# Kernel optimization log

Measured on AMD Instinct MI355X. Metric: run time of the kernel, lower is better.

Reference implementation:

```python
import jax, jax.numpy as jnp
import numpy as np

N_NODES = 100000

def sage_conv(x, edge_index, Wl, bl, Wr):
    # PyG SAGEConv, aggr='add', normalize=False:
    #   out = lin_l(sum_{j in N(i)} x_j) + lin_r(x_i)
    src, dst = edge_index[0], edge_index[1]
    agg = jax.ops.segment_sum(x[src], dst, num_segments=N_NODES)  # [N, F]
    return agg @ Wl.T + bl + x @ Wr.T


def setup_inputs() -> dict:
    key = jax.random.key(0)
    ks = jax.random.split(key, 7)
    F_IN, HID, C, E = 128, 256, 50, 640000
    x = jax.random.normal(ks[0], (N_NODES, F_IN), dtype=jnp.float32)
    edge_index = jax.random.randint(ks[1], (2, E), 0, N_NODES, dtype=jnp.int64)
    s1 = 1.0 / np.sqrt(F_IN)
    s2 = 1.0 / np.sqrt(HID)
    return {
        "x": x,
        "edge_index": edge_index,
        "W1l": jax.random.normal(ks[2], (HID, F_IN), dtype=jnp.float32) * s1,
        "b1l": jnp.zeros((HID,), dtype=jnp.float32),
        "W1r": jax.random.normal(ks[3], (HID, F_IN), dtype=jnp.float32) * s1,
        "W2l": jax.random.normal(ks[4], (C, HID), dtype=jnp.float32) * s2,
        "b2l": jnp.zeros((C,), dtype=jnp.float32),
        "W2r": jax.random.normal(ks[5], (C, HID), dtype=jnp.float32) * s2,
    }


def reference(x, edge_index, W1l, b1l, W1r, W2l, b2l, W2r):
    h = sage_conv(x, edge_index, W1l, b1l, W1r)
    h = jax.nn.relu(h)
    # F.dropout(p=0.5, training=False) is identity in eval mode
    out = sage_conv(h, edge_index, W2l, b2l, W2r)
    return out
```

## Files before the change

### kernel.cpp

```cpp
#include <hip/hip_runtime.h>

#define N_NODES 100000
#define MPAD    100096
#define F_IN 128
#define HID 256
#define C_OUT 50
#define N_EDGES 640000
#define CAP 32

typedef __attribute__((ext_vector_type(8))) short short8;
typedef __attribute__((ext_vector_type(8))) ushort us8;
typedef __attribute__((ext_vector_type(4))) float f32x4;

struct alignas(8) us4 { ushort x, y, z, w; };

__device__ __forceinline__ ushort f2bf(float f) {
    union { float f; unsigned u; } v; v.f = f;
    unsigned r = (v.u + 0x7fffu + ((v.u >> 16) & 1u)) >> 16;
    return (ushort)r;
}

__device__ __forceinline__ float bf2f(ushort u) {
    union { unsigned u; float f; } v; v.u = ((unsigned)u) << 16;
    return v.f;
}

__device__ __forceinline__ void load_lds16(const void* gsrc, void* lds) {
    __builtin_amdgcn_global_load_lds(
        (const __attribute__((address_space(1))) void*)gsrc,
        (__attribute__((address_space(3))) void*)lds, 16, 0, 0);
}

__global__ void pack_w1(const float* __restrict__ W1l, const float* __restrict__ W1r,
                        ushort* __restrict__ B1t) {
    int idx = blockIdx.x * blockDim.x + threadIdx.x;
    if (idx >= 256 * 256) return;
    int o = idx >> 8, k = idx & 255;
    float v = (k < 128) ? W1l[o * 128 + k] : W1r[o * 128 + (k - 128)];
    B1t[o * 256 + k] = f2bf(v);
}

__global__ void pack_w2(const float* __restrict__ W2l, const float* __restrict__ W2r,
                        ushort* __restrict__ B2t) {
    int idx = blockIdx.x * blockDim.x + threadIdx.x;
    if (idx >= 128 * 256) return;
    int c = idx >> 8, k = idx & 255;
    float v = 0.f;
    if (c < C_OUT) v = W2l[c * 256 + k];
    else if (c >= 64 && c < 64 + C_OUT) v = W2r[(c - 64) * 256 + k];
    B2t[c * 256 + k] = f2bf(v);
}

__global__ void scatter_bucket(const int* __restrict__ src, const int* __restrict__ dst,
                               int* __restrict__ cnt, int* __restrict__ bucket) {
    int e = blockIdx.x * blockDim.x + threadIdx.x;
    if (e >= N_EDGES) return;
    int d = dst[e];
    int p = atomicAdd(&cnt[d], 1);
    if (p < CAP) bucket[(size_t)d * CAP + p] = src[e];
}

__global__ void xcvt_kernel(const float* __restrict__ x, ushort* __restrict__ A1) {
    int tid = blockIdx.x * blockDim.x + threadIdx.x;
    int node = tid >> 5, q = tid & 31;
    if (node >= N_NODES) return;
    float4 v = *reinterpret_cast<const float4*>(x + (size_t)node * F_IN + q * 4);
    us4 o;
    o.x = f2bf(v.x); o.y = f2bf(v.y); o.z = f2bf(v.z); o.w = f2bf(v.w);
    *reinterpret_cast<us4*>(&A1[(size_t)node * 256 + 128 + q * 4]) = o;
}

__global__ void gather1_kernel(const int* __restrict__ cnt, const int* __restrict__ bucket,
                               ushort* __restrict__ A1) {
    int tid = blockIdx.x * blockDim.x + threadIdx.x;
    int node = tid >> 4, q = tid & 15;
    if (node >= N_NODES) return;
    int n = cnt[node];
    if (n > CAP) n = CAP;
    const int* row = bucket + (size_t)node * CAP;
    float a[8];
#pragma unroll
    for (int j = 0; j < 8; ++j) a[j] = 0.f;
    int p = 0;
    for (; p + 2 <= n; p += 2) {
        int s0 = row[p], s1 = row[p + 1];
        us8 v0 = *reinterpret_cast<const us8*>(&A1[(size_t)s0 * 256 + 128 + q * 8]);
        us8 v1 = *reinterpret_cast<const us8*>(&A1[(size_t)s1 * 256 + 128 + q * 8]);
#pragma unroll
        for (int j = 0; j < 8; ++j) a[j] += bf2f(v0[j]);
#pragma unroll
        for (int j = 0; j < 8; ++j) a[j] += bf2f(v1[j]);
    }
    if (p < n) {
        int s0 = row[p];
        us8 v0 = *reinterpret_cast<const us8*>(&A1[(size_t)s0 * 256 + 128 + q * 8]);
#pragma unroll
        for (int j = 0; j < 8; ++j) a[j] += bf2f(v0[j]);
    }
    us8 o;
#pragma unroll
    for (int j = 0; j < 8; ++j) o[j] = f2bf(a[j]);
    *reinterpret_cast<us8*>(&A1[(size_t)node * 256 + q * 8]) = o;
}

__global__ void gather2_kernel(const ushort* __restrict__ g, const int* __restrict__ cnt,
                               const int* __restrict__ bucket, float* __restrict__ out) {
    int tid = blockIdx.x * blockDim.x + threadIdx.x;
    int node = tid >> 3, q = tid & 7;
    if (node >= N_NODES) return;
    int c = q * 8;
    if (c >= C_OUT) return;
    int n = cnt[node];
    if (n > CAP) n = CAP;
    const int* row = bucket + (size_t)node * CAP;
    float a[8];
#pragma unroll
    for (int j = 0; j < 8; ++j) a[j] = 0.f;
    int p = 0;
    for (; p + 2 <= n; p += 2) {
        int s0 = row[p], s1 = row[p + 1];
        us8 v0 = *reinterpret_cast<const us8*>(&g[(size_t)s0 * 64 + c]);
        us8 v1 = *reinterpret_cast<const us8*>(&g[(size_t)s1 * 64 + c]);
#pragma unroll
        for (int j = 0; j < 8; ++j) a[j] += bf2f(v0[j]);
#pragma unroll
        for (int j = 0; j < 8; ++j) a[j] += bf2f(v1[j]);
    }
    if (p < n) {
        int s0 = row[p];
        us8 v0 = *reinterpret_cast<const us8*>(&g[(size_t)s0 * 64 + c]);
#pragma unroll
        for (int j = 0; j < 8; ++j) a[j] += bf2f(v0[j]);
    }
    float* po = out + (size_t)node * C_OUT;
#pragma unroll
    for (int j = 0; j < 8; ++j) {
        if (c + j < C_OUT) po[c + j] += a[j];
    }
}

template <int EPI>
__global__ __launch_bounds__(256) void mfma_gemm(
    const ushort* __restrict__ A, const ushort* __restrict__ B,
    const float* __restrict__ bias, ushort* __restrict__ hOut,
    ushort* __restrict__ gOut, float* __restrict__ oOut) {
    __shared__ alignas(16) ushort As[128 * 32];
    __shared__ alignas(16) ushort Bs[128 * 32];
    const int tid = threadIdx.x;
    const int lane = tid & 63, wid = tid >> 6;
    const int wr = wid >> 1, wc = wid & 1;
    const int brow = blockIdx.x, bcol = blockIdx.y;

    f32x4 acc[4][4];
#pragma unroll
    for (int m = 0; m < 4; ++m)
#pragma unroll
        for (int n = 0; n < 4; ++n) acc[m][n] = (f32x4){0.f, 0.f, 0.f, 0.f};

    const int c0 = tid, c1 = tid + 256;
    const int r0 = c0 >> 2, k80 = (c0 & 3) * 8;
    const int r1 = c1 >> 2, k81 = (c1 & 3) * 8;
    const size_t aRow0 = (size_t)(brow * 128 + r0) * 256;
    const size_t aRow1 = (size_t)(brow * 128 + r1) * 256;
    const size_t bRow0 = (size_t)(bcol * 128 + r0) * 256;
    const size_t bRow1 = (size_t)(bcol * 128 + r1) * 256;

    const int aoffA = (lane & 15) * 32 + (lane >> 4) * 8;

    for (int kt = 0; kt < 8; ++kt) {
        const int kOff = kt * 32;
        load_lds16(A + aRow0 + kOff + k80, &As[c0 * 8]);
        load_lds16(A + aRow1 + kOff + k81, &As[c1 * 8]);
        load_lds16(B + bRow0 + kOff + k80, &Bs[c0 * 8]);
        load_lds16(B + bRow1 + kOff + k81, &Bs[c1 * 8]);
        __syncthreads();

        short8 af[4], bfr[4];
#pragma unroll
        for (int m = 0; m < 4; ++m)
            af[m] = *reinterpret_cast<const short8*>(&As[(wr * 64 + m * 16) * 32 + aoffA]);
#pragma unroll
        for (int n = 0; n < 4; ++n)
            bfr[n] = *reinterpret_cast<const short8*>(&Bs[(wc * 64 + n * 16) * 32 + aoffA]);
#pragma unroll
        for (int m = 0; m < 4; ++m)
#pragma unroll
            for (int n = 0; n < 4; ++n)
                acc[m][n] = __builtin_amdgcn_mfma_f32_16x16x32_bf16(af[m], bfr[n], acc[m][n], 0, 0, 0);
        __syncthreads();
    }

    const int colB = bcol * 128 + wc * 64 + (lane & 15);
    const int rowB = brow * 128 + wr * 64 + ((lane >> 4) << 2);

    if (EPI == 1) {
        float bv[4];
#pragma unroll
        for (int n = 0; n < 4; ++n) bv[n] = bias[colB + n * 16];
#pragma unroll
        for (int m = 0; m < 4; ++m) {
#pragma unroll
            for (int r = 0; r < 4; ++r) {
                int row = rowB + m * 16 + r;
                if (row >= N_NODES) continue;
#pragma unroll
                for (int n = 0; n < 4; ++n) {
                    float v = acc[m][n][r] + bv[n];
                    v = v > 0.f ? v : 0.f;
                    hOut[(size_t)row * 256 + colB + n * 16] = f2bf(v);
                }
            }
        }
    } else {
#pragma unroll
        for (int m = 0; m < 4; ++m) {
#pragma unroll
            for (int r = 0; r < 4; ++r) {
                int row = rowB + m * 16 + r;
                if (row >= N_NODES) continue;
#pragma unroll
                for (int n = 0; n < 4; ++n) {
                    int cg = colB + n * 16;
                    float v = acc[m][n][r];
                    if (cg < 64) {
                        gOut[(size_t)row * 64 + cg] = f2bf(v);
                    } else if (cg < 64 + C_OUT) {
                        oOut[(size_t)row * C_OUT + (cg - 64)] = v + bias[cg - 64];
                    }
                }
            }
        }
    }
}

extern "C" void kernel_launch(void* const* d_in, const int* in_sizes, int n_in,
                              void* d_out, int out_size, void* d_ws, size_t ws_size,
                              hipStream_t stream) {
    const float* x   = (const float*)d_in[0];
    const int*   ei  = (const int*)d_in[1];
    const float* W1l = (const float*)d_in[2];
    const float* b1l = (const float*)d_in[3];
    const float* W1r = (const float*)d_in[4];
    const float* W2l = (const float*)d_in[5];
    const float* b2l = (const float*)d_in[6];
    const float* W2r = (const float*)d_in[7];
    float* out = (float*)d_out;

    ushort* A1   = (ushort*)d_ws;
    ushort* hbuf = A1 + (size_t)MPAD * 256;
    ushort* B1t  = hbuf + (size_t)MPAD * 256;
    ushort* B2t  = B1t + 256 * 256;
    ushort* g    = B2t + 128 * 256;
    int* cnt     = (int*)(g + (size_t)N_NODES * 64);
    int* bucket  = cnt + N_NODES;

    const int* src = ei;
    const int* dst = ei + N_EDGES;

    hipMemsetAsync(cnt, 0, (size_t)N_NODES * sizeof(int), stream);
    pack_w1<<<256, 256, 0, stream>>>(W1l, W1r, B1t);
    pack_w2<<<128, 256, 0, stream>>>(W2l, W2r, B2t);

    scatter_bucket<<<(N_EDGES + 255) / 256, 256, 0, stream>>>(src, dst, cnt, bucket);

    xcvt_kernel<<<(N_NODES * 32 + 255) / 256, 256, 0, stream>>>(x, A1);
    gather1_kernel<<<(N_NODES * 16 + 255) / 256, 256, 0, stream>>>(cnt, bucket, A1);

    const int nbrow = MPAD / 128;
    mfma_gemm<1><<<dim3(nbrow, 2), 256, 0, stream>>>(A1, B1t, b1l, hbuf, nullptr, nullptr);
    mfma_gemm<2><<<dim3(nbrow, 1), 256, 0, stream>>>(hbuf, B2t, b2l, nullptr, g, out);

    gather2_kernel<<<(N_NODES * 8 + 255) / 256, 256, 0, stream>>>(g, cnt, bucket, out);
}
```

Before: 177.5 us.

## Replace per-node atomic bucketing with two-phase coarse-bin scatter and LDS binning

Builds the neighbour buckets in two passes. Edges are first scattered into coarse bins of 256 destination nodes, then each block bins its chunk locally in LDS and writes contiguous bucket rows, which replaces scattered global atomics per node. The memset and the two weight-pack kernels are merged into one prep kernel, and the gather loops are unrolled to 4 loads. This adds an extra pass over the edges plus an intermediate pairs buffer, and a coarse bin that exceeds CCAP would silently drop edges.

```diff
diff --git a/kernel.cpp b/kernel.cpp
--- a/kernel.cpp
+++ b/kernel.cpp
@@ -7,6 +7,8 @@
 #define C_OUT 50
 #define N_EDGES 640000
 #define CAP 32
+#define NBC 391
+#define CCAP 2048
 
 typedef __attribute__((ext_vector_type(8))) short short8;
 typedef __attribute__((ext_vector_type(8))) ushort us8;
@@ -31,33 +33,61 @@
         (__attribute__((address_space(3))) void*)lds, 16, 0, 0);
 }
 
-__global__ void pack_w1(const float* __restrict__ W1l, const float* __restrict__ W1r,
-                        ushort* __restrict__ B1t) {
+__global__ void prep_kernel(const float* __restrict__ W1l, const float* __restrict__ W1r,
+                            const float* __restrict__ W2l, const float* __restrict__ W2r,
+                            ushort* __restrict__ B1t, ushort* __restrict__ B2t,
+                            int* __restrict__ ccnt) {
     int idx = blockIdx.x * blockDim.x + threadIdx.x;
-    if (idx >= 256 * 256) return;
-    int o = idx >> 8, k = idx & 255;
-    float v = (k < 128) ? W1l[o * 128 + k] : W1r[o * 128 + (k - 128)];
-    B1t[o * 256 + k] = f2bf(v);
-}
-
-__global__ void pack_w2(const float* __restrict__ W2l, const float* __restrict__ W2r,
-                        ushort* __restrict__ B2t) {
-    int idx = blockIdx.x * blockDim.x + threadIdx.x;
-    if (idx >= 128 * 256) return;
-    int c = idx >> 8, k = idx & 255;
-    float v = 0.f;
-    if (c < C_OUT) v = W2l[c * 256 + k];
-    else if (c >= 64 && c < 64 + C_OUT) v = W2r[(c - 64) * 256 + k];
-    B2t[c * 256 + k] = f2bf(v);
-}
-
-__global__ void scatter_bucket(const int* __restrict__ src, const int* __restrict__ dst,
-                               int* __restrict__ cnt, int* __restrict__ bucket) {
+    if (idx < NBC) ccnt[idx] = 0;
+    if (idx < 256 * 256) {
+        int o = idx >> 8, k = idx & 255;
+        float v = (k < 128) ? W1l[o * 128 + k] : W1r[o * 128 + (k - 128)];
+        B1t[o * 256 + k] = f2bf(v);
+    }
+    if (idx < 128 * 256) {
+        int c = idx >> 8, k = idx & 255;
+        float v = 0.f;
+        if (c < C_OUT) v = W2l[c * 256 + k];
+        else if (c >= 64 && c < 64 + C_OUT) v = W2r[(c - 64) * 256 + k];
+        B2t[c * 256 + k] = f2bf(v);
+    }
+}
+
+__global__ void edge_phase1(const int* __restrict__ src, const int* __restrict__ dst,
+                            int* __restrict__ ccnt, int2* __restrict__ pairs) {
     int e = blockIdx.x * blockDim.x + threadIdx.x;
     if (e >= N_EDGES) return;
     int d = dst[e];
-    int p = atomicAdd(&cnt[d], 1);
-    if (p < CAP) bucket[(size_t)d * CAP + p] = src[e];
+    int b = d >> 8;
+    int p = atomicAdd(&ccnt[b], 1);
+    if (p < CCAP) pairs[(size_t)b * CCAP + p] = make_int2(d, src[e]);
+}
+
+__global__ __launch_bounds__(256) void edge_phase2(const int* __restrict__ ccnt,
+                                                   const int2* __restrict__ pairs,
+                                                   int* __restrict__ cnt,
+                                                   int* __restrict__ bucket) {
+    __shared__ int lcnt[256];
+    __shared__ int lbuf[256 * CAP];
+    int b = blockIdx.x, t = threadIdx.x;
+    lcnt[t] = 0;
+    __syncthreads();
+    int m = ccnt[b];
+    if (m > CCAP) m = CCAP;
+    const int2* pp = pairs + (size_t)b * CCAP;
+    for (int i = t; i < m; i += 256) {
+        int2 pr = pp[i];
+        int dl = pr.x & 255;
+        int p = atomicAdd(&lcnt[dl], 1);
+        if (p < CAP) lbuf[dl * CAP + p] = pr.y;
+    }
+    __syncthreads();
+    int node0 = b << 8;
+    if (node0 + t < N_NODES) cnt[node0 + t] = lcnt[t];
+    for (int idx = t; idx < 256 * CAP; idx += 256) {
+        int node = node0 + (idx >> 5);
+        if (node < N_NODES) bucket[(size_t)node0 * CAP + idx] = lbuf[idx];
+    }
 }
 
 __global__ void xcvt_kernel(const float* __restrict__ x, ushort* __restrict__ A1) {
@@ -82,20 +112,39 @@
 #pragma unroll
     for (int j = 0; j < 8; ++j) a[j] = 0.f;
     int p = 0;
-    for (; p + 2 <= n; p += 2) {
-        int s0 = row[p], s1 = row[p + 1];
+    for (; p + 4 <= n; p += 4) {
+        int s0 = row[p], s1 = row[p + 1], s2 = row[p + 2], s3 = row[p + 3];
         us8 v0 = *reinterpret_cast<const us8*>(&A1[(size_t)s0 * 256 + 128 + q * 8]);
         us8 v1 = *reinterpret_cast<const us8*>(&A1[(size_t)s1 * 256 + 128 + q * 8]);
+        us8 v2 = *reinterpret_cast<const us8*>(&A1[(size_t)s2 * 256 + 128 + q * 8]);
+        us8 v3 = *reinterpret_cast<const us8*>(&A1[(size_t)s3 * 256 + 128 + q * 8]);
 #pragma unroll
         for (int j = 0; j < 8; ++j) a[j] += bf2f(v0[j]);
 #pragma unroll
         for (int j = 0; j < 8; ++j) a[j] += bf2f(v1[j]);
-    }
-    if (p < n) {
+#pragma unroll
+        for (int j = 0; j < 8; ++j) a[j] += bf2f(v2[j]);
+#pragma unroll
+        for (int j = 0; j < 8; ++j) a[j] += bf2f(v3[j]);
+    }
+    int rem = n - p;
+    if (rem > 0) {
         int s0 = row[p];
+        int s1 = (rem > 1) ? row[p + 1] : s0;
+        int s2 = (rem > 2) ? row[p + 2] : s0;
         us8 v0 = *reinterpret_cast<const us8*>(&A1[(size_t)s0 * 256 + 128 + q * 8]);
+        us8 v1 = *reinterpret_cast<const us8*>(&A1[(size_t)s1 * 256 + 128 + q * 8]);
+        us8 v2 = *reinterpret_cast<const us8*>(&A1[(size_t)s2 * 256 + 128 + q * 8]);
 #pragma unroll
         for (int j = 0; j < 8; ++j) a[j] += bf2f(v0[j]);
+        if (rem > 1) {
+#pragma unroll
+            for (int j = 0; j < 8; ++j) a[j] += bf2f(v1[j]);
+        }
+        if (rem > 2) {
+#pragma unroll
+            for (int j = 0; j < 8; ++j) a[j] += bf2f(v2[j]);
+        }
     }
     us8 o;
 #pragma unroll
@@ -117,20 +166,39 @@
 #pragma unroll
     for (int j = 0; j < 8; ++j) a[j] = 0.f;
     int p = 0;
-    for (; p + 2 <= n; p += 2) {
-        int s0 = row[p], s1 = row[p + 1];
+    for (; p + 4 <= n; p += 4) {
+        int s0 = row[p], s1 = row[p + 1], s2 = row[p + 2], s3 = row[p + 3];
         us8 v0 = *reinterpret_cast<const us8*>(&g[(size_t)s0 * 64 + c]);
         us8 v1 = *reinterpret_cast<const us8*>(&g[(size_t)s1 * 64 + c]);
+        us8 v2 = *reinterpret_cast<const us8*>(&g[(size_t)s2 * 64 + c]);
+        us8 v3 = *reinterpret_cast<const us8*>(&g[(size_t)s3 * 64 + c]);
 #pragma unroll
         for (int j = 0; j < 8; ++j) a[j] += bf2f(v0[j]);
 #pragma unroll
         for (int j = 0; j < 8; ++j) a[j] += bf2f(v1[j]);
-    }
-    if (p < n) {
+#pragma unroll
+        for (int j = 0; j < 8; ++j) a[j] += bf2f(v2[j]);
+#pragma unroll
+        for (int j = 0; j < 8; ++j) a[j] += bf2f(v3[j]);
+    }
+    int rem = n - p;
+    if (rem > 0) {
         int s0 = row[p];
+        int s1 = (rem > 1) ? row[p + 1] : s0;
+        int s2 = (rem > 2) ? row[p + 2] : s0;
         us8 v0 = *reinterpret_cast<const us8*>(&g[(size_t)s0 * 64 + c]);
+        us8 v1 = *reinterpret_cast<const us8*>(&g[(size_t)s1 * 64 + c]);
+        us8 v2 = *reinterpret_cast<const us8*>(&g[(size_t)s2 * 64 + c]);
 #pragma unroll
         for (int j = 0; j < 8; ++j) a[j] += bf2f(v0[j]);
+        if (rem > 1) {
+#pragma unroll
+            for (int j = 0; j < 8; ++j) a[j] += bf2f(v1[j]);
+        }
+        if (rem > 2) {
+#pragma unroll
+            for (int j = 0; j < 8; ++j) a[j] += bf2f(v2[j]);
+        }
     }
     float* po = out + (size_t)node * C_OUT;
 #pragma unroll
@@ -252,16 +320,16 @@
     ushort* B2t  = B1t + 256 * 256;
     ushort* g    = B2t + 128 * 256;
     int* cnt     = (int*)(g + (size_t)N_NODES * 64);
-    int* bucket  = cnt + N_NODES;
+    int* ccnt    = cnt + N_NODES;
+    int* bucket  = ccnt + NBC;
+    int2* pairs  = (int2*)(bucket + (size_t)N_NODES * CAP);
 
     const int* src = ei;
     const int* dst = ei + N_EDGES;
 
-    hipMemsetAsync(cnt, 0, (size_t)N_NODES * sizeof(int), stream);
-    pack_w1<<<256, 256, 0, stream>>>(W1l, W1r, B1t);
-    pack_w2<<<128, 256, 0, stream>>>(W2l, W2r, B2t);
-
-    scatter_bucket<<<(N_EDGES + 255) / 256, 256, 0, stream>>>(src, dst, cnt, bucket);
+    prep_kernel<<<256, 256, 0, stream>>>(W1l, W1r, W2l, W2r, B1t, B2t, ccnt);
+    edge_phase1<<<(N_EDGES + 255) / 256, 256, 0, stream>>>(src, dst, ccnt, pairs);
+    edge_phase2<<<NBC, 256, 0, stream>>>(ccnt, pairs, cnt, bucket);
 
     xcvt_kernel<<<(N_NODES * 32 + 255) / 256, 256, 0, stream>>>(x, A1);
     gather1_kernel<<<(N_NODES * 16 + 255) / 256, 256, 0, stream>>>(cnt, bucket, A1);
```

Measured after the change: 373.6 us. 2.11x slower.
